# Optimization experiments

Hardware: AMD Instinct MI355X
Metric: run time of the kernel (lower is better)

The kernel has to match this reference:

```python
import jax, jax.numpy as jnp
import numpy as np

B, D_IN, N_EXP, D_EXP, TOP_K = 8192, 1024, 8, 1024, 2


def setup_inputs() -> dict:
    key = jax.random.key(0)
    ks = jax.random.split(key, 6)
    s_in = 1.0 / np.sqrt(D_IN)
    s_exp = 1.0 / np.sqrt(D_EXP)
    return {
        "x": jax.random.normal(ks[0], (B, D_IN), jnp.float32),
        "gate_w": jax.random.normal(ks[1], (D_IN, N_EXP), jnp.float32) * s_in,
        "w1": jax.random.normal(ks[2], (N_EXP, D_IN, D_EXP), jnp.float32) * s_in,
        "b1": jax.random.normal(ks[3], (N_EXP, D_EXP), jnp.float32) * 0.01,
        "w2": jax.random.normal(ks[4], (N_EXP, D_EXP, D_EXP), jnp.float32) * s_exp,
        "b2": jax.random.normal(ks[5], (N_EXP, D_EXP), jnp.float32) * 0.01,
    }


def _moe(x, gate_w, w1, b1, w2, b2):
    # Gating: top-k sparse softmax over expert logits.
    gate_logits = x @ gate_w                          # (B, E)
    top_vals, top_idx = jax.lax.top_k(gate_logits, TOP_K)  # (B, K)
    # softmax over only the top-k logits == softmax of -inf-scattered logits
    top_w = jax.nn.softmax(top_vals, axis=-1)          # (B, K)
    gate_weights = jnp.zeros_like(gate_logits).at[
        jnp.arange(x.shape[0])[:, None], top_idx
    ].set(top_w)                                       # (B, E)
    # Dense all-expert MLP (matches torch.stack over experts).
    h = jax.nn.gelu(jnp.einsum("bd,edf->ebf", x, w1) + b1[:, None, :],
                    approximate=False)                 # (E, B, F)
    expert_outs = jnp.einsum("ebf,efg->ebg", h, w2) + b2[:, None, :]  # (E, B, G)
    output = jnp.einsum("be,ebg->bg", gate_weights, expert_outs)      # (B, G)
    return output, gate_weights


def reference(x, gate_w, w1, b1, w2, b2):
    return _moe(x, gate_w, w1, b1, w2, b2)
```

## Files before the change

kernel.cpp:

```cpp
#include <hip/hip_runtime.h>
#include <math.h>
#include <stdint.h>


#define NTOK   8192
#define DIN    1024
#define NEXP   8
#define DEXP   1024
#define MAXROWS 18432
#define MAXT   72

typedef __bf16 bf16x8_t __attribute__((ext_vector_type(8)));
typedef float f32x4 __attribute__((ext_vector_type(4)));

__device__ __forceinline__ unsigned short f2bf(float f) {
  union { float f; unsigned int u; } v; v.f = f;
  unsigned int u = v.u;
  u += 0x7fffu + ((u >> 16) & 1u);
  return (unsigned short)(u >> 16);
}

__device__ __forceinline__ float bf2f(unsigned short s) {
  union { unsigned int u; float f; } v; v.u = ((unsigned int)s) << 16;
  return v.f;
}

__device__ __forceinline__ void async16(const void* g, void* l) {
  __builtin_amdgcn_global_load_lds((const __attribute__((address_space(1))) void*)g,
                                   (__attribute__((address_space(3))) void*)l, 16, 0, 0);
}

__device__ __forceinline__ float gelu_fast(float v) {
  float u = v * (1.5957691216057308f + 0.07135481627f * v * v);
  return v * (1.0f / (1.0f + __expf(-u)));
}

__global__ __launch_bounds__(256) void gate_cast_kernel(const float* __restrict__ x,
                                                        const float* __restrict__ gw,
                                                        const float* __restrict__ w2,
                                                        unsigned short* __restrict__ xbf,
                                                        unsigned short* __restrict__ w2T,
                                                        float* __restrict__ outGate,
                                                        int* __restrict__ topE,
                                                        float* __restrict__ topW,
                                                        int* __restrict__ rowTok) {
  __shared__ __align__(16) char smem[32768];
  int b = blockIdx.x;
  int tid = threadIdx.x;
  if (b >= 4096) {
    int base = (b - 4096) * 1024 + tid * 4;
    *(int4*)(rowTok + base) = make_int4(-1, -1, -1, -1);
    return;
  }
  if (b >= 2048) {
    float* tile = (float*)smem;
    int idx = b - 2048;
    int e = idx >> 8, rest = idx & 255, kt = rest >> 4, nt = rest & 15;
    const float* s = w2 + (size_t)e * DEXP * DEXP + (size_t)kt * 64 * 1024 + nt * 64;
    unsigned short* d = w2T + (size_t)e * DEXP * DEXP + (size_t)nt * 64 * 1024 + kt * 64;
    int a = tid & 15, r0 = tid >> 4;
    #pragma unroll
    for (int p = 0; p < 4; ++p) {
      int r = r0 + p * 16;
      float4 v = *(const float4*)(s + (size_t)r * 1024 + a * 4);
      tile[r * 65 + a * 4 + 0] = v.x;
      tile[r * 65 + a * 4 + 1] = v.y;
      tile[r * 65 + a * 4 + 2] = v.z;
      tile[r * 65 + a * 4 + 3] = v.w;
    }
    __syncthreads();
    #pragma unroll
    for (int p = 0; p < 4; ++p) {
      int nr = r0 + p * 16;
      ushort4 o;
      o.x = f2bf(tile[(a * 4 + 0) * 65 + nr]);
      o.y = f2bf(tile[(a * 4 + 1) * 65 + nr]);
      o.z = f2bf(tile[(a * 4 + 2) * 65 + nr]);
      o.w = f2bf(tile[(a * 4 + 3) * 65 + nr]);
      *(ushort4*)(d + (size_t)nr * 1024 + a * 4) = o;
    }
    return;
  }
  float (*gwT)[1024] = (float(*)[1024])smem;
  #pragma unroll
  for (int it = 0; it < 8; ++it) {
    int idx = it * 256 + tid;
    int fk = idx >> 1;
    int e0 = (idx & 1) * 4;
    float4 g = *(const float4*)(gw + fk * 8 + e0);
    gwT[e0 + 0][fk] = g.x; gwT[e0 + 1][fk] = g.y;
    gwT[e0 + 2][fk] = g.z; gwT[e0 + 3][fk] = g.w;
  }
  __syncthreads();

  int lane = tid & 63, wv = tid >> 6;
  int t = b * 4 + wv;
  const float4* xr = (const float4*)(x + (size_t)t * 1024);
  ushort4* xo = (ushort4*)(xbf + (size_t)t * 1024);
  double acc[NEXP];
  #pragma unroll
  for (int e = 0; e < NEXP; ++e) acc[e] = 0.0;
  #pragma unroll
  for (int j = 0; j < 4; ++j) {
    int q = lane + 64 * j;
    float4 v = xr[q];
    ushort4 r;
    r.x = f2bf(v.x); r.y = f2bf(v.y); r.z = f2bf(v.z); r.w = f2bf(v.w);
    xo[q] = r;
    float vv[4] = {v.x, v.y, v.z, v.w};
    #pragma unroll
    for (int e = 0; e < NEXP; ++e) {
      float4 g = *(const float4*)&gwT[e][4 * q];
      acc[e] += (double)vv[0] * (double)g.x;
      acc[e] += (double)vv[1] * (double)g.y;
      acc[e] += (double)vv[2] * (double)g.z;
      acc[e] += (double)vv[3] * (double)g.w;
    }
  }
  #pragma unroll
  for (int off = 32; off > 0; off >>= 1) {
    #pragma unroll
    for (int e = 0; e < NEXP; ++e) acc[e] += __shfl_xor(acc[e], off);
  }
  if (lane == 0) {
    int e0 = 0; double v0 = acc[0];
    #pragma unroll
    for (int e = 1; e < NEXP; ++e) if (acc[e] > v0) { v0 = acc[e]; e0 = e; }
    int e1 = -1; double v1 = -1e300;
    #pragma unroll
    for (int e = 0; e < NEXP; ++e) if (e != e0 && acc[e] > v1) { v1 = acc[e]; e1 = e; }
    float ex = expf((float)(v1 - v0));
    float inv = 1.0f / (1.0f + ex);
    float w0 = inv, w1v = ex * inv;
    float g8[8];
    #pragma unroll
    for (int e = 0; e < NEXP; ++e) g8[e] = 0.f;
    g8[e0] = w0; g8[e1] = w1v;
    float4* gp = (float4*)(outGate + t * 8);
    gp[0] = *(float4*)&g8[0];
    gp[1] = *(float4*)&g8[4];
    topE[t * 2 + 0] = e0; topE[t * 2 + 1] = e1;
    topW[t * 2 + 0] = w0; topW[t * 2 + 1] = w1v;
  }
}

__global__ __launch_bounds__(1024) void slot_kernel(const int* __restrict__ topE,
                                                    int* __restrict__ topRow,
                                                    int* __restrict__ rowTok,
                                                    int* __restrict__ tileExpert,
                                                    int* __restrict__ tileRowBase,
                                                    const float* __restrict__ w1,
                                                    unsigned short* __restrict__ w1T) {
  __shared__ int wtot[16][NEXP];
  __shared__ int wbase[16][NEXP];
  __shared__ int soff[NEXP];
  __shared__ float tile[64 * 65];
  int tid = threadIdx.x;
  if (blockIdx.x != 0) {
    int idx = blockIdx.x - 1;
    int e = idx >> 8, rest = idx & 255, kt = rest >> 4, nt = rest & 15;
    const float* s = w1 + (size_t)e * DIN * DEXP + (size_t)kt * 64 * 1024 + nt * 64;
    unsigned short* d = w1T + (size_t)e * DIN * DEXP + (size_t)nt * 64 * 1024 + kt * 64;
    int a = tid & 15, r = tid >> 4;
    float4 v = *(const float4*)(s + (size_t)r * 1024 + a * 4);
    tile[r * 65 + a * 4 + 0] = v.x;
    tile[r * 65 + a * 4 + 1] = v.y;
    tile[r * 65 + a * 4 + 2] = v.z;
    tile[r * 65 + a * 4 + 3] = v.w;
    __syncthreads();
    int nr = r;
    ushort4 o;
    o.x = f2bf(tile[(a * 4 + 0) * 65 + nr]);
    o.y = f2bf(tile[(a * 4 + 1) * 65 + nr]);
    o.z = f2bf(tile[(a * 4 + 2) * 65 + nr]);
    o.w = f2bf(tile[(a * 4 + 3) * 65 + nr]);
    *(ushort4*)(d + (size_t)nr * 1024 + a * 4) = o;
    return;
  }
  int lane = tid & 63, wv = tid >> 6;
  int a0 = tid * 16;
  unsigned long long pk = 0ull;
  int cnt[NEXP];
  #pragma unroll
  for (int e = 0; e < NEXP; ++e) cnt[e] = 0;
  for (int i = 0; i < 16; ++i) {
    int e = topE[a0 + i];
    pk |= (unsigned long long)e << (i * 4);
    cnt[e]++;
  }
  int excl[NEXP];
  #pragma unroll
  for (int e = 0; e < NEXP; ++e) {
    int v = cnt[e], sum = v;
    #pragma unroll
    for (int d = 1; d < 64; d <<= 1) {
      int u = __shfl_up(sum, d);
      if (lane >= d) sum += u;
    }
    excl[e] = sum - v;
    if (lane == 63) wtot[wv][e] = sum;
  }
  __syncthreads();
  if (tid == 0) {
    int counts[NEXP];
    for (int e = 0; e < NEXP; ++e) {
      int s = 0;
      for (int w = 0; w < 16; ++w) { wbase[w][e] = s; s += wtot[w][e]; }
      counts[e] = s;
    }
    int row = 0, tl = 0;
    for (int e = 0; e < NEXP; ++e) {
      soff[e] = row;
      int nt = (counts[e] + 255) >> 8;
      for (int i = 0; i < nt; ++i) { tileExpert[tl] = e; tileRowBase[tl] = row + i * 256; ++tl; }
      row += nt << 8;
    }
    for (; tl < MAXT; ++tl) tileExpert[tl] = -1;
  }
  __syncthreads();
  int base[NEXP], run[NEXP];
  #pragma unroll
  for (int e = 0; e < NEXP; ++e) { base[e] = soff[e] + wbase[wv][e] + excl[e]; run[e] = 0; }
  for (int i = 0; i < 16; ++i) {
    int e = (int)((pk >> (i * 4)) & 7ull);
    int row = base[e] + run[e]++;
    rowTok[row] = (a0 + i) >> 1;
    topRow[a0 + i] = row;
  }
}

template <bool GATHER, bool GELU>
__global__ __launch_bounds__(512, 2) void moe_gemm_kernel(
    const unsigned short* __restrict__ Asrc,
    const unsigned short* __restrict__ Wt,
    const float* __restrict__ bias,
    const int* __restrict__ tileExpert,
    const int* __restrict__ tileRowBase,
    const int* __restrict__ rowTok,
    unsigned short* __restrict__ Out) {
  int e = tileExpert[blockIdx.x];
  if (e < 0) return;
  int rowBase = tileRowBase[blockIdx.x];
  int n0 = blockIdx.y * 256;
  __shared__ __align__(16) unsigned short sm[65536];

  int tid = threadIdx.x;
  int lane = tid & 63, wq = tid >> 6;
  int wr = wq >> 2, wc = wq & 3;
  int rsel = lane & 15, qq = (lane >> 4) & 3, rk = rsel & 7;
  int sid = tid >> 3, sch = tid & 7;
  int swz8 = (sch ^ (sid & 7)) * 8;

  int arow[4];
  #pragma unroll
  for (int j = 0; j < 4; ++j) {
    int r = rowBase + j * 64 + sid;
    if (GATHER) { int tk = rowTok[r]; arow[j] = tk < 0 ? 0 : tk; }
    else arow[j] = r;
  }
  const unsigned short* Bsrc = Wt + (size_t)e * 1024 * 1024;

  auto stage = [&](int T) {
    int kk_ = T * 64;
    int sel_ = (T & 1) * 32768;
    #pragma unroll
    for (int j = 0; j < 4; ++j) {
      int ab = __builtin_amdgcn_readfirstlane(sel_ + j * 8192 + wq * 1024);
      async16(Asrc + (size_t)arow[j] * 1024 + kk_ + swz8, (char*)sm + ab);
      async16(Bsrc + (size_t)(n0 + j * 64 + sid) * 1024 + kk_ + swz8,
              (char*)sm + 65536 + ab);
    }
  };

  f32x4 acc[8][4] = {};

  stage(0);
  stage(1);
  asm volatile("s_waitcnt vmcnt(8)" ::: "memory");
  __builtin_amdgcn_s_barrier();

  for (int t = 0; t < 16; ++t) {
    int sel = (t & 1) * 32768;
    const unsigned short* sA = (const unsigned short*)((const char*)sm + sel);
    const unsigned short* sB = (const unsigned short*)((const char*)sm + 65536 + sel);
    bf16x8_t bfr[4][2];
    #pragma unroll
    for (int ni = 0; ni < 4; ++ni)
      #pragma unroll
      for (int ks = 0; ks < 2; ++ks)
        bfr[ni][ks] = *(const bf16x8_t*)
            &sB[(wc * 64 + ni * 16 + rsel) * 64 + ((qq + 4 * ks) ^ rk) * 8];
    #pragma unroll
    for (int p = 0; p < 4; ++p) {
      bf16x8_t af[2][2];
      #pragma unroll
      for (int d = 0; d < 2; ++d)
        #pragma unroll
        for (int ks = 0; ks < 2; ++ks)
          af[d][ks] = *(const bf16x8_t*)
              &sA[(wr * 128 + (p * 2 + d) * 16 + rsel) * 64 + ((qq + 4 * ks) ^ rk) * 8];
      __builtin_amdgcn_s_barrier();
      __builtin_amdgcn_s_setprio(1);
      #pragma unroll
      for (int d = 0; d < 2; ++d)
        #pragma unroll
        for (int ni = 0; ni < 4; ++ni)
          #pragma unroll
          for (int ks = 0; ks < 2; ++ks)
            acc[p * 2 + d][ni] = __builtin_amdgcn_mfma_f32_16x16x32_bf16(
                af[d][ks], bfr[ni][ks], acc[p * 2 + d][ni], 0, 0, 0);
      __builtin_amdgcn_s_setprio(0);
      __builtin_amdgcn_s_barrier();
    }
    if (t + 2 < 16) {
      stage(t + 2);
      asm volatile("s_waitcnt vmcnt(8)" ::: "memory");
    } else {
      asm volatile("s_waitcnt vmcnt(0)" ::: "memory");
    }
    __builtin_amdgcn_s_barrier();
  }

  __syncthreads();
  float bv[4];
  #pragma unroll
  for (int ni = 0; ni < 4; ++ni)
    bv[ni] = bias[e * 1024 + n0 + wc * 64 + ni * 16 + rsel];
  #pragma unroll
  for (int mi = 0; mi < 8; ++mi)
    #pragma unroll
    for (int ni = 0; ni < 4; ++ni)
      #pragma unroll
      for (int r = 0; r < 4; ++r) {
        int m = wr * 128 + mi * 16 + qq * 4 + r;
        int n = wc * 64 + ni * 16 + rsel;
        float v = acc[mi][ni][r] + bv[ni];
        if (GELU) v = gelu_fast(v);
        sm[m * 256 + n] = f2bf(v);
      }
  __syncthreads();
  #pragma unroll
  for (int i = 0; i < 16; ++i) {
    int idx = i * 8192 + tid * 16;
    int m = idx >> 9, cb = idx & 511;
    *(uint4*)(Out + (size_t)(rowBase + m) * 1024 + n0 + (cb >> 1)) =
        *(const uint4*)((const char*)sm + idx);
  }
}

__global__ __launch_bounds__(256) void combine_kernel(const unsigned short* __restrict__ y,
                                                      const int* __restrict__ topRow,
                                                      const float* __restrict__ topW,
                                                      float* __restrict__ out) {
  int tid = threadIdx.x;
  int wv = tid >> 6, lane = tid & 63;
  int t = blockIdx.x * 4 + wv;
  int r0 = topRow[t * 2 + 0], r1 = topRow[t * 2 + 1];
  float w0 = topW[t * 2 + 0], w1 = topW[t * 2 + 1];
  const unsigned short* p0 = y + (size_t)r0 * 1024 + lane * 16;
  const unsigned short* p1 = y + (size_t)r1 * 1024 + lane * 16;
  float* op = out + (size_t)t * 1024 + lane * 16;
  #pragma unroll
  for (int hh = 0; hh < 2; ++hh) {
    union { uint4 v; unsigned short s[8]; } a, b;
    a.v = *(const uint4*)(p0 + hh * 8);
    b.v = *(const uint4*)(p1 + hh * 8);
    float o[8];
    #pragma unroll
    for (int j = 0; j < 8; ++j)
      o[j] = w0 * bf2f(a.s[j]) + w1 * bf2f(b.s[j]);
    *(float4*)(op + hh * 8) = *(float4*)&o[0];
    *(float4*)(op + hh * 8 + 4) = *(float4*)&o[4];
  }
}

extern "C" void kernel_launch(void* const* d_in, const int* in_sizes, int n_in,
                              void* d_out, int out_size, void* d_ws, size_t ws_size,
                              hipStream_t stream) {
  const float* x  = (const float*)d_in[0];
  const float* gw = (const float*)d_in[1];
  const float* w1 = (const float*)d_in[2];
  const float* b1 = (const float*)d_in[3];
  const float* w2 = (const float*)d_in[4];
  const float* b2 = (const float*)d_in[5];
  float* out = (float*)d_out;

  char* ws = (char*)d_ws;
  int* tileExpert  = (int*)ws;
  int* tileRowBase = tileExpert + MAXT;
  int* topE        = tileRowBase + MAXT;
  int* topRow      = topE + 16384;
  float* topW      = (float*)(topRow + 16384);
  int* rowTok      = (int*)(ws + (256 << 10));
  unsigned short* xbf  = (unsigned short*)(ws + (512 << 10));
  unsigned short* w1T  = xbf + (size_t)NTOK * DIN;
  unsigned short* w2T  = w1T + (size_t)NEXP * DIN * DEXP;
  unsigned short* hbuf = w2T + (size_t)NEXP * DEXP * DEXP;
  unsigned short* ybuf = hbuf + (size_t)MAXROWS * DEXP;

  gate_cast_kernel<<<2048 + 2048 + 18, 256, 0, stream>>>(x, gw, w2, xbf, w2T,
                                                         out + (size_t)NTOK * DEXP,
                                                         topE, topW, rowTok);
  slot_kernel<<<1 + 2048, 1024, 0, stream>>>(topE, topRow, rowTok, tileExpert,
                                             tileRowBase, w1, w1T);
  moe_gemm_kernel<true, true><<<dim3(MAXT, 4), 512, 0, stream>>>(
      xbf, w1T, b1, tileExpert, tileRowBase, rowTok, hbuf);
  moe_gemm_kernel<false, false><<<dim3(MAXT, 4), 512, 0, stream>>>(
      hbuf, w2T, b2, tileExpert, tileRowBase, rowTok, ybuf);
  combine_kernel<<<NTOK / 4, 256, 0, stream>>>(ybuf, topRow, topW, out);
}
```

Before: 322.9 us.

## Shrink MoE GEMM tiles to 128x128 with 4-wave blocks and swapped grid axes

Reworks the grouped expert GEMM from 256x256 output tiles with 512 threads and BK=64 into 128x128 tiles with 256 threads and BK=32. The slot kernel now emits twice as many 128-row tiles per expert, and the grid is transposed so column blocks vary fastest. The intent is more blocks in flight and better occupancy, since 144x8 blocks give more parallelism across the 256 CUs than 72x4. In exchange, arithmetic intensity per LDS byte and per global load drops, and each block runs more k-iterations with barriers.

```diff
diff --git a/kernel.cpp b/kernel.cpp
--- a/kernel.cpp
+++ b/kernel.cpp
@@ -8,7 +8,7 @@
 #define NEXP   8
 #define DEXP   1024
 #define MAXROWS 18432
-#define MAXT   72
+#define MAXT   144
 
 typedef __bf16 bf16x8_t __attribute__((ext_vector_type(8)));
 typedef float f32x4 __attribute__((ext_vector_type(4)));
@@ -211,9 +211,11 @@
     int row = 0, tl = 0;
     for (int e = 0; e < NEXP; ++e) {
       soff[e] = row;
-      int nt = (counts[e] + 255) >> 8;
-      for (int i = 0; i < nt; ++i) { tileExpert[tl] = e; tileRowBase[tl] = row + i * 256; ++tl; }
-      row += nt << 8;
+      int nt256 = (counts[e] + 255) >> 8;
+      for (int i = 0; i < nt256 * 2; ++i) {
+        tileExpert[tl] = e; tileRowBase[tl] = row + i * 128; ++tl;
+      }
+      row += nt256 << 8;
     }
     for (; tl < MAXT; ++tl) tileExpert[tl] = -1;
   }
@@ -230,7 +232,7 @@
 }
 
 template <bool GATHER, bool GELU>
-__global__ __launch_bounds__(512, 2) void moe_gemm_kernel(
+__global__ __launch_bounds__(256, 4) void moe_gemm_kernel(
     const unsigned short* __restrict__ Asrc,
     const unsigned short* __restrict__ Wt,
     const float* __restrict__ bias,
@@ -238,111 +240,96 @@
     const int* __restrict__ tileRowBase,
     const int* __restrict__ rowTok,
     unsigned short* __restrict__ Out) {
-  int e = tileExpert[blockIdx.x];
+  int e = tileExpert[blockIdx.y];
   if (e < 0) return;
-  int rowBase = tileRowBase[blockIdx.x];
-  int n0 = blockIdx.y * 256;
-  __shared__ __align__(16) unsigned short sm[65536];
+  int rowBase = tileRowBase[blockIdx.y];
+  int n0 = blockIdx.x * 128;
+  __shared__ __align__(16) unsigned short sm[16384];
 
   int tid = threadIdx.x;
-  int lane = tid & 63, wq = tid >> 6;
-  int wr = wq >> 2, wc = wq & 3;
-  int rsel = lane & 15, qq = (lane >> 4) & 3, rk = rsel & 7;
-  int sid = tid >> 3, sch = tid & 7;
-  int swz8 = (sch ^ (sid & 7)) * 8;
-
-  int arow[4];
-  #pragma unroll
-  for (int j = 0; j < 4; ++j) {
-    int r = rowBase + j * 64 + sid;
+  int lane = tid & 63, wv = tid >> 6;
+  int wr = wv >> 1, wc = wv & 1;
+  int rsel = lane & 15, q = (lane >> 4) & 3, rk = rsel & 3;
+  int sr = tid >> 2;
+  int swz = ((tid & 3) ^ (sr & 3)) * 8;
+
+  int arow[2];
+  #pragma unroll
+  for (int j = 0; j < 2; ++j) {
+    int r = rowBase + j * 64 + sr;
     if (GATHER) { int tk = rowTok[r]; arow[j] = tk < 0 ? 0 : tk; }
     else arow[j] = r;
   }
   const unsigned short* Bsrc = Wt + (size_t)e * 1024 * 1024;
 
   auto stage = [&](int T) {
-    int kk_ = T * 64;
-    int sel_ = (T & 1) * 32768;
-    #pragma unroll
-    for (int j = 0; j < 4; ++j) {
-      int ab = __builtin_amdgcn_readfirstlane(sel_ + j * 8192 + wq * 1024);
-      async16(Asrc + (size_t)arow[j] * 1024 + kk_ + swz8, (char*)sm + ab);
-      async16(Bsrc + (size_t)(n0 + j * 64 + sid) * 1024 + kk_ + swz8,
-              (char*)sm + 65536 + ab);
+    int kk = T * 32;
+    int selB = (T & 1) * 16384;
+    #pragma unroll
+    for (int j = 0; j < 2; ++j) {
+      int ab = __builtin_amdgcn_readfirstlane(selB + j * 4096 + wv * 1024);
+      async16(Asrc + (size_t)arow[j] * 1024 + kk + swz, (char*)sm + ab);
+      async16(Bsrc + (size_t)(n0 + j * 64 + sr) * 1024 + kk + swz,
+              (char*)sm + ab + 8192);
     }
   };
 
-  f32x4 acc[8][4] = {};
+  f32x4 acc[4][4] = {};
 
   stage(0);
   stage(1);
-  asm volatile("s_waitcnt vmcnt(8)" ::: "memory");
+  asm volatile("s_waitcnt vmcnt(4)" ::: "memory");
   __builtin_amdgcn_s_barrier();
 
-  for (int t = 0; t < 16; ++t) {
-    int sel = (t & 1) * 32768;
-    const unsigned short* sA = (const unsigned short*)((const char*)sm + sel);
-    const unsigned short* sB = (const unsigned short*)((const char*)sm + 65536 + sel);
-    bf16x8_t bfr[4][2];
+  for (int t = 0; t < 32; ++t) {
+    const unsigned short* sA = sm + (t & 1) * 8192;
+    const unsigned short* sB = sA + 4096;
+    bf16x8_t af[4], bf[4];
+    #pragma unroll
+    for (int mi = 0; mi < 4; ++mi)
+      af[mi] = *(const bf16x8_t*)&sA[(wr * 64 + mi * 16 + rsel) * 32 + (q ^ rk) * 8];
     #pragma unroll
     for (int ni = 0; ni < 4; ++ni)
+      bf[ni] = *(const bf16x8_t*)&sB[(wc * 64 + ni * 16 + rsel) * 32 + (q ^ rk) * 8];
+    __builtin_amdgcn_s_setprio(1);
+    #pragma unroll
+    for (int mi = 0; mi < 4; ++mi)
       #pragma unroll
-      for (int ks = 0; ks < 2; ++ks)
-        bfr[ni][ks] = *(const bf16x8_t*)
-            &sB[(wc * 64 + ni * 16 + rsel) * 64 + ((qq + 4 * ks) ^ rk) * 8];
-    #pragma unroll
-    for (int p = 0; p < 4; ++p) {
-      bf16x8_t af[2][2];
-      #pragma unroll
-      for (int d = 0; d < 2; ++d)
-        #pragma unroll
-        for (int ks = 0; ks < 2; ++ks)
-          af[d][ks] = *(const bf16x8_t*)
-              &sA[(wr * 128 + (p * 2 + d) * 16 + rsel) * 64 + ((qq + 4 * ks) ^ rk) * 8];
-      __builtin_amdgcn_s_barrier();
-      __builtin_amdgcn_s_setprio(1);
-      #pragma unroll
-      for (int d = 0; d < 2; ++d)
-        #pragma unroll
-        for (int ni = 0; ni < 4; ++ni)
-          #pragma unroll
-          for (int ks = 0; ks < 2; ++ks)
-            acc[p * 2 + d][ni] = __builtin_amdgcn_mfma_f32_16x16x32_bf16(
-                af[d][ks], bfr[ni][ks], acc[p * 2 + d][ni], 0, 0, 0);
-      __builtin_amdgcn_s_setprio(0);
-      __builtin_amdgcn_s_barrier();
-    }
-    if (t + 2 < 16) {
+      for (int ni = 0; ni < 4; ++ni)
+        acc[mi][ni] = __builtin_amdgcn_mfma_f32_16x16x32_bf16(af[mi], bf[ni], acc[mi][ni], 0, 0, 0);
+    __builtin_amdgcn_s_setprio(0);
+    __builtin_amdgcn_s_barrier();
+    if (t + 2 < 32) {
       stage(t + 2);
-      asm volatile("s_waitcnt vmcnt(8)" ::: "memory");
+      asm volatile("s_waitcnt vmcnt(4)" ::: "memory");
     } else {
       asm volatile("s_waitcnt vmcnt(0)" ::: "memory");
     }
     __builtin_amdgcn_s_barrier();
   }
 
-  __syncthreads();
   float bv[4];
+  int quad = lane >> 4;
   #pragma unroll
   for (int ni = 0; ni < 4; ++ni)
     bv[ni] = bias[e * 1024 + n0 + wc * 64 + ni * 16 + rsel];
   #pragma unroll
-  for (int mi = 0; mi < 8; ++mi)
+  for (int mi = 0; mi < 4; ++mi)
     #pragma unroll
     for (int ni = 0; ni < 4; ++ni)
       #pragma unroll
       for (int r = 0; r < 4; ++r) {
-        int m = wr * 128 + mi * 16 + qq * 4 + r;
+        int m = wr * 64 + mi * 16 + quad * 4 + r;
         int n = wc * 64 + ni * 16 + rsel;
         float v = acc[mi][ni][r] + bv[ni];
         if (GELU) v = gelu_fast(v);
-        sm[m * 256 + n] = f2bf(v);
+        sm[m * 128 + n] = f2bf(v);
       }
   __syncthreads();
   #pragma unroll
-  for (int i = 0; i < 16; ++i) {
-    int idx = i * 8192 + tid * 16;
-    int m = idx >> 9, cb = idx & 511;
+  for (int i = 0; i < 8; ++i) {
+    int idx = i * 4096 + tid * 16;
+    int m = idx >> 8, cb = idx & 255;
     *(uint4*)(Out + (size_t)(rowBase + m) * 1024 + n0 + (cb >> 1)) =
         *(const uint4*)((const char*)sm + idx);
   }
@@ -403,9 +390,9 @@
                                                          topE, topW, rowTok);
   slot_kernel<<<1 + 2048, 1024, 0, stream>>>(topE, topRow, rowTok, tileExpert,
                                              tileRowBase, w1, w1T);
-  moe_gemm_kernel<true, true><<<dim3(MAXT, 4), 512, 0, stream>>>(
+  moe_gemm_kernel<true, true><<<dim3(8, MAXT), 256, 0, stream>>>(
       xbf, w1T, b1, tileExpert, tileRowBase, rowTok, hbuf);
-  moe_gemm_kernel<false, false><<<dim3(MAXT, 4), 512, 0, stream>>>(
+  moe_gemm_kernel<false, false><<<dim3(8, MAXT), 256, 0, stream>>>(
       hbuf, w2T, b2, tileExpert, tileRowBase, rowTok, ybuf);
   combine_kernel<<<NTOK / 4, 256, 0, stream>>>(ybuf, topRow, topW, out);
 }
```

Result: faster. 296.6 us (-8.1%).
